# Optimization experiments

Measured on AMD Instinct MI355X. Metric: run time of the kernel, lower is better.

The kernel has to match this reference:

```python
import jax, jax.numpy as jnp
import numpy as np

NUM_CLASSES = 1000
SCALE = 1.0

def setup_inputs() -> dict:
    key = jax.random.key(0)
    x = jax.random.normal(key, (32768, NUM_CLASSES), dtype=jnp.float32)
    return {"input": x}

def reference(input) -> jnp.ndarray:
    # residual defaults to input in the torch module
    r = input                                   # [B, C]
    n = NUM_CLASSES
    ra = jnp.abs(r)
    mean = jnp.mean(ra, axis=-1, keepdims=True)
    std = jnp.std(ra, axis=-1, keepdims=True, ddof=1)  # torch.std is unbiased
    w = SCALE * jax.nn.sigmoid((ra - mean) / std)       # [B, C]
    # W = I + 1/(n-1) * diag(w) @ (ones - n*I);  (W r)_i = r_i + w_i/(n-1)*(sum(r) - n*r_i)
    s = jnp.sum(r, axis=-1, keepdims=True)              # [B, 1]
    out = r + w / (n - 1) * (s - n * r)
    return out
```

## Files before the change

kernel.cpp:

```cpp
#include <hip/hip_runtime.h>
#include <math.h>

#define NC   1000
#define NVEC 250
#define WPB  4
#define RPW  4
#define L2E  1.4426950408889634f

typedef float v4f __attribute__((ext_vector_type(4)));

#if __has_builtin(__builtin_amdgcn_exp2f)
#define FAST_EXP2(x) __builtin_amdgcn_exp2f(x)
#else
#define FAST_EXP2(x) exp2f(x)
#endif

#if __has_builtin(__builtin_amdgcn_rcpf)
#define FAST_RCP(x) __builtin_amdgcn_rcpf(x)
#else
#define FAST_RCP(x) (1.0f / (x))
#endif

struct Row { float4 c0, c1, c2, c3; };

__device__ __forceinline__ Row load_row(const float* __restrict__ in, int row,
                                        int lane, bool tail) {
    const float4* __restrict__ rp = (const float4*)(in + (size_t)row * NC);
    Row r;
    r.c0 = rp[lane];
    r.c1 = rp[lane + 64];
    r.c2 = rp[lane + 128];
    r.c3 = tail ? rp[lane + 192] : make_float4(0.f, 0.f, 0.f, 0.f);
    return r;
}

__device__ __forceinline__ void accum_chunk(const float4& c, float& sr, float& sa, float& sa2) {
    const float a0 = fabsf(c.x), a1 = fabsf(c.y), a2 = fabsf(c.z), a3 = fabsf(c.w);
    sr  += (c.x + c.y) + (c.z + c.w);
    sa  += (a0 + a1) + (a2 + a3);
    sa2 += (a0 * a0 + a1 * a1) + (a2 * a2 + a3 * a3);
}

__device__ __forceinline__ float elem(float x, float kx, float bx, float cn, float cS) {
    return fmaf(FAST_RCP(1.0f + FAST_EXP2(fmaf(fabsf(x), kx, bx))), fmaf(-cn, x, cS), x);
}

__device__ __forceinline__ void do_epilogue(const Row& r, float S, float SA, float SA2,
                                            float* __restrict__ out, int row,
                                            int lane, bool tail) {
    const float mean    = SA * (1.0f / NC);
    const float var     = (SA2 - (float)NC * mean * mean) * (1.0f / (NC - 1));
    const float inv_std = rsqrtf(var);
    const float kx = -inv_std * L2E;
    const float bx =  mean * inv_std * L2E;
    const float c  = 1.0f / (NC - 1);
    const float cS = c * S;
    const float cn = c * (float)NC;

    v4f* __restrict__ op = (v4f*)(out + (size_t)row * NC);
    {
        v4f o;
        o.x = elem(r.c0.x, kx, bx, cn, cS);
        o.y = elem(r.c0.y, kx, bx, cn, cS);
        o.z = elem(r.c0.z, kx, bx, cn, cS);
        o.w = elem(r.c0.w, kx, bx, cn, cS);
        __builtin_nontemporal_store(o, &op[lane]);
    }
    {
        v4f o;
        o.x = elem(r.c1.x, kx, bx, cn, cS);
        o.y = elem(r.c1.y, kx, bx, cn, cS);
        o.z = elem(r.c1.z, kx, bx, cn, cS);
        o.w = elem(r.c1.w, kx, bx, cn, cS);
        __builtin_nontemporal_store(o, &op[lane + 64]);
    }
    {
        v4f o;
        o.x = elem(r.c2.x, kx, bx, cn, cS);
        o.y = elem(r.c2.y, kx, bx, cn, cS);
        o.z = elem(r.c2.z, kx, bx, cn, cS);
        o.w = elem(r.c2.w, kx, bx, cn, cS);
        __builtin_nontemporal_store(o, &op[lane + 128]);
    }
    if (tail) {
        v4f o;
        o.x = elem(r.c3.x, kx, bx, cn, cS);
        o.y = elem(r.c3.y, kx, bx, cn, cS);
        o.z = elem(r.c3.z, kx, bx, cn, cS);
        o.w = elem(r.c3.w, kx, bx, cn, cS);
        __builtin_nontemporal_store(o, &op[lane + 192]);
    }
}

__global__ __launch_bounds__(256, 4)
void smooth_filter_kernel(const float* __restrict__ in,
                          float* __restrict__ out,
                          int rows) {
    const int  lane = threadIdx.x & 63;
    const bool tail = (lane < (NVEC - 192));
    const int  wid  = blockIdx.x * WPB + (threadIdx.x >> 6);
    const int  row0 = wid * RPW;
    if (row0 >= rows) return;

    const bool h1 = (row0 + 1) < rows;
    const bool h2 = (row0 + 2) < rows;
    const bool h3 = (row0 + 3) < rows;

    Row A0 = load_row(in, row0, lane, tail);
    Row A1, B0, B1;
    if (h1) A1 = load_row(in, row0 + 1, lane, tail); else A1 = A0;
    if (h2) B0 = load_row(in, row0 + 2, lane, tail); else B0 = A0;
    if (h3) B1 = load_row(in, row0 + 3, lane, tail); else B1 = A0;

    {
        float xr = 0.f, xa = 0.f, xa2 = 0.f;
        float yr = 0.f, ya = 0.f, ya2 = 0.f;
        accum_chunk(A0.c0, xr, xa, xa2);
        accum_chunk(A0.c1, xr, xa, xa2);
        accum_chunk(A0.c2, xr, xa, xa2);
        accum_chunk(A0.c3, xr, xa, xa2);
        accum_chunk(A1.c0, yr, ya, ya2);
        accum_chunk(A1.c1, yr, ya, ya2);
        accum_chunk(A1.c2, yr, ya, ya2);
        accum_chunk(A1.c3, yr, ya, ya2);

        #pragma unroll
        for (int off = 32; off > 0; off >>= 1) {
            xr  += __shfl_xor(xr,  off, 64);
            yr  += __shfl_xor(yr,  off, 64);
            xa  += __shfl_xor(xa,  off, 64);
            ya  += __shfl_xor(ya,  off, 64);
            xa2 += __shfl_xor(xa2, off, 64);
            ya2 += __shfl_xor(ya2, off, 64);
        }

        do_epilogue(A0, xr, xa, xa2, out, row0, lane, tail);
        if (h1) do_epilogue(A1, yr, ya, ya2, out, row0 + 1, lane, tail);
    }

    {
        float xr = 0.f, xa = 0.f, xa2 = 0.f;
        float yr = 0.f, ya = 0.f, ya2 = 0.f;
        accum_chunk(B0.c0, xr, xa, xa2);
        accum_chunk(B0.c1, xr, xa, xa2);
        accum_chunk(B0.c2, xr, xa, xa2);
        accum_chunk(B0.c3, xr, xa, xa2);
        accum_chunk(B1.c0, yr, ya, ya2);
        accum_chunk(B1.c1, yr, ya, ya2);
        accum_chunk(B1.c2, yr, ya, ya2);
        accum_chunk(B1.c3, yr, ya, ya2);

        #pragma unroll
        for (int off = 32; off > 0; off >>= 1) {
            xr  += __shfl_xor(xr,  off, 64);
            yr  += __shfl_xor(yr,  off, 64);
            xa  += __shfl_xor(xa,  off, 64);
            ya  += __shfl_xor(ya,  off, 64);
            xa2 += __shfl_xor(xa2, off, 64);
            ya2 += __shfl_xor(ya2, off, 64);
        }

        if (h2) do_epilogue(B0, xr, xa, xa2, out, row0 + 2, lane, tail);
        if (h3) do_epilogue(B1, yr, ya, ya2, out, row0 + 3, lane, tail);
    }
}

extern "C" void kernel_launch(void* const* d_in, const int* in_sizes, int n_in,
                              void* d_out, int out_size, void* d_ws, size_t ws_size,
                              hipStream_t stream) {
    const float* in  = (const float*)d_in[0];
    float*       out = (float*)d_out;
    const int rows   = in_sizes[0] / NC;
    const int rpb    = WPB * RPW;
    const int blocks = (rows + rpb - 1) / rpb;
    smooth_filter_kernel<<<blocks, 256, 0, stream>>>(in, out, rows);
}
```

Measured before the change: 229.5 us.

## Software-pipeline row loads with one-row lookahead and eight rows per wave

Replaces the up-front load of four rows with a rolling double buffer: each wave prefetches the next row while it reduces and writes the current one, and now handles eight rows per wave. This lowers register pressure from four live rows to two and is meant to overlap global loads with compute. The catch is less memory-level parallelism per wave, since only one row load is in flight at a time, and half as many blocks in the grid.

Result: slower. 238.2 us (+3.8%).

```diff
diff --git a/kernel.cpp b/kernel.cpp
--- a/kernel.cpp
+++ b/kernel.cpp
@@ -4,7 +4,7 @@
 #define NC   1000
 #define NVEC 250
 #define WPB  4
-#define RPW  4
+#define RPW  8
 #define L2E  1.4426950408889634f
 
 typedef float v4f __attribute__((ext_vector_type(4)));
@@ -45,16 +45,28 @@
     return fmaf(FAST_RCP(1.0f + FAST_EXP2(fmaf(fabsf(x), kx, bx))), fmaf(-cn, x, cS), x);
 }
 
-__device__ __forceinline__ void do_epilogue(const Row& r, float S, float SA, float SA2,
-                                            float* __restrict__ out, int row,
-                                            int lane, bool tail) {
-    const float mean    = SA * (1.0f / NC);
-    const float var     = (SA2 - (float)NC * mean * mean) * (1.0f / (NC - 1));
+__device__ __forceinline__ void process_row(const Row& r, float* __restrict__ out,
+                                            int row, int lane, bool tail) {
+    float sr = 0.f, sa = 0.f, sa2 = 0.f;
+    accum_chunk(r.c0, sr, sa, sa2);
+    accum_chunk(r.c1, sr, sa, sa2);
+    accum_chunk(r.c2, sr, sa, sa2);
+    accum_chunk(r.c3, sr, sa, sa2);
+
+    #pragma unroll
+    for (int off = 32; off > 0; off >>= 1) {
+        sr  += __shfl_xor(sr,  off, 64);
+        sa  += __shfl_xor(sa,  off, 64);
+        sa2 += __shfl_xor(sa2, off, 64);
+    }
+
+    const float mean    = sa * (1.0f / NC);
+    const float var     = (sa2 - (float)NC * mean * mean) * (1.0f / (NC - 1));
     const float inv_std = rsqrtf(var);
     const float kx = -inv_std * L2E;
     const float bx =  mean * inv_std * L2E;
     const float c  = 1.0f / (NC - 1);
-    const float cS = c * S;
+    const float cS = c * sr;
     const float cn = c * (float)NC;
 
     v4f* __restrict__ op = (v4f*)(out + (size_t)row * NC);
@@ -102,66 +114,25 @@
     const int  row0 = wid * RPW;
     if (row0 >= rows) return;
 
-    const bool h1 = (row0 + 1) < rows;
-    const bool h2 = (row0 + 2) < rows;
-    const bool h3 = (row0 + 3) < rows;
-
-    Row A0 = load_row(in, row0, lane, tail);
-    Row A1, B0, B1;
-    if (h1) A1 = load_row(in, row0 + 1, lane, tail); else A1 = A0;
-    if (h2) B0 = load_row(in, row0 + 2, lane, tail); else B0 = A0;
-    if (h3) B1 = load_row(in, row0 + 3, lane, tail); else B1 = A0;
-
-    {
-        float xr = 0.f, xa = 0.f, xa2 = 0.f;
-        float yr = 0.f, ya = 0.f, ya2 = 0.f;
-        accum_chunk(A0.c0, xr, xa, xa2);
-        accum_chunk(A0.c1, xr, xa, xa2);
-        accum_chunk(A0.c2, xr, xa, xa2);
-        accum_chunk(A0.c3, xr, xa, xa2);
-        accum_chunk(A1.c0, yr, ya, ya2);
-        accum_chunk(A1.c1, yr, ya, ya2);
-        accum_chunk(A1.c2, yr, ya, ya2);
-        accum_chunk(A1.c3, yr, ya, ya2);
-
+    if (row0 + RPW <= rows) {
+        Row cur = load_row(in, row0, lane, tail);
         #pragma unroll
-        for (int off = 32; off > 0; off >>= 1) {
-            xr  += __shfl_xor(xr,  off, 64);
-            yr  += __shfl_xor(yr,  off, 64);
-            xa  += __shfl_xor(xa,  off, 64);
-            ya  += __shfl_xor(ya,  off, 64);
-            xa2 += __shfl_xor(xa2, off, 64);
-            ya2 += __shfl_xor(ya2, off, 64);
+        for (int r = 0; r < RPW; ++r) {
+            Row nxt;
+            if (r + 1 < RPW) nxt = load_row(in, row0 + r + 1, lane, tail);
+            process_row(cur, out, row0 + r, lane, tail);
+            if (r + 1 < RPW) cur = nxt;
         }
-
-        do_epilogue(A0, xr, xa, xa2, out, row0, lane, tail);
-        if (h1) do_epilogue(A1, yr, ya, ya2, out, row0 + 1, lane, tail);
-    }
-
-    {
-        float xr = 0.f, xa = 0.f, xa2 = 0.f;
-        float yr = 0.f, ya = 0.f, ya2 = 0.f;
-        accum_chunk(B0.c0, xr, xa, xa2);
-        accum_chunk(B0.c1, xr, xa, xa2);
-        accum_chunk(B0.c2, xr, xa, xa2);
-        accum_chunk(B0.c3, xr, xa, xa2);
-        accum_chunk(B1.c0, yr, ya, ya2);
-        accum_chunk(B1.c1, yr, ya, ya2);
-        accum_chunk(B1.c2, yr, ya, ya2);
-        accum_chunk(B1.c3, yr, ya, ya2);
-
+    } else {
+        Row cur = load_row(in, row0, lane, tail);
         #pragma unroll
-        for (int off = 32; off > 0; off >>= 1) {
-            xr  += __shfl_xor(xr,  off, 64);
-            yr  += __shfl_xor(yr,  off, 64);
-            xa  += __shfl_xor(xa,  off, 64);
-            ya  += __shfl_xor(ya,  off, 64);
-            xa2 += __shfl_xor(xa2, off, 64);
-            ya2 += __shfl_xor(ya2, off, 64);
+        for (int r = 0; r < RPW; ++r) {
+            const bool hn = (row0 + r + 1 < rows) && (r + 1 < RPW);
+            Row nxt;
+            if (hn) nxt = load_row(in, row0 + r + 1, lane, tail);
+            process_row(cur, out, row0 + r, lane, tail);
+            if (hn) cur = nxt; else break;
         }
-
-        if (h2) do_epilogue(B0, xr, xa, xa2, out, row0 + 2, lane, tail);
-        if (h3) do_epilogue(B1, yr, ya, ya2, out, row0 + 3, lane, tail);
     }
 }
 
```
